# Kernel optimization log

Measured on AMD Instinct MI355X. Metric: run time of the kernel, lower is better.

## Reference

```python
import math
import jax, jax.numpy as jnp
import numpy as np

N_HEADS = 16
THETA = 10000.0


def _rope_cos_sin(S, head_dim):
    half = head_dim // 2
    inv_freq = 1.0 / (THETA ** (jnp.arange(half, dtype=jnp.float32) / half))
    t = jnp.arange(S, dtype=jnp.float32)
    freqs = t[:, None] * inv_freq[None, :]  # [S, half]
    return jnp.cos(freqs), jnp.sin(freqs)


def _apply_rope(x, cos, sin):
    # x: [B, H, S, D] float32; cos/sin: [S, D//2]
    half = x.shape[-1] // 2
    x1, x2 = x[..., :half], x[..., half:]
    c = cos[None, None, :, :]
    s = sin[None, None, :, :]
    return jnp.concatenate([x1 * c - x2 * s, x1 * s + x2 * c], axis=-1)


def setup_inputs() -> dict:
    key = jax.random.key(0)
    k1, k2, k3 = jax.random.split(key, 3)
    B, S, D = 4, 2048, 1024
    x = jax.random.normal(k1, (B, S, D), dtype=jnp.float32)
    w_qkv = jax.random.normal(k2, (3 * D, D), dtype=jnp.float32) * (1.0 / math.sqrt(D))
    w_out = jax.random.normal(k3, (D, D), dtype=jnp.float32) * (1.0 / math.sqrt(D))
    return {"x": x, "w_qkv": w_qkv, "w_out": w_out}


def reference(x, w_qkv, w_out):
    B, S, D = x.shape
    H = N_HEADS
    hd = D // H

    qkv = x @ w_qkv.T  # [B, S, 3D]
    q, k, v = jnp.split(qkv, 3, axis=-1)

    def reshape(t):
        return t.reshape(B, S, H, hd).transpose(0, 2, 1, 3)  # [B,H,S,hd]

    q, k, v = reshape(q), reshape(k), reshape(v)

    cos, sin = _rope_cos_sin(S, hd)
    q = _apply_rope(q.astype(jnp.float32), cos, sin).astype(x.dtype)
    k = _apply_rope(k.astype(jnp.float32), cos, sin).astype(x.dtype)

    scale = math.sqrt(hd)
    scores = jnp.einsum("bhsd,bhtd->bhst", q, k) / scale  # [B,H,S,S]
    causal = jnp.tril(jnp.ones((S, S), dtype=bool))
    scores = jnp.where(causal[None, None], scores, -jnp.inf)
    attn = jax.nn.softmax(scores.astype(jnp.float32), axis=-1).astype(x.dtype)

    out = jnp.einsum("bhst,bhtd->bhsd", attn, v)  # [B,H,S,hd]
    out = out.transpose(0, 2, 1, 3).reshape(B, S, D)
    return out @ w_out.T
```

## Files before the change

kernel.cpp:

```cpp
#include <hip/hip_runtime.h>
#include <hip/hip_bf16.h>

#define DEV static __device__ __forceinline__

typedef unsigned short u16;
typedef unsigned int u32;
typedef __attribute__((ext_vector_type(8))) short short8;
typedef __attribute__((ext_vector_type(4))) float f32x4;
typedef __attribute__((ext_vector_type(16))) float f32x16;
typedef __attribute__((ext_vector_type(4))) u32 u32x4;

static constexpr int Bsz = 4, Ssz = 2048, Dsz = 1024, Hn = 16, HD = 64;
static constexpr int Mrows = Bsz * Ssz;

DEV u16 f2bu(float f) {
  union { float f; u32 u; } a; a.f = f;
  u32 u = a.u;
  u32 r = (u + 0x7FFFu + ((u >> 16) & 1u)) >> 16;
  return (u16)r;
}
DEV float b2f(u16 v) {
  union { u32 u; float f; } a; a.u = ((u32)v) << 16;
  return a.f;
}
DEV u32 pk2(float lo, float hi2) {
  __hip_bfloat162 t = __float22bfloat162_rn(make_float2(lo, hi2));
  u32 r; __builtin_memcpy(&r, &t, 4); return r;
}
DEV f32x16 mfma3232(short8 a, short8 b, f32x16 c) {
  return __builtin_amdgcn_mfma_f32_32x32x16_bf16(a, b, c, 0, 0, 0);
}
DEV float max3f(float a, float b, float c) { return fmaxf(fmaxf(a, b), c); }
DEV float ex2(float x) { return __builtin_amdgcn_exp2f(x); }

__global__ void k_cast(const float4* __restrict__ in, ushort4* __restrict__ out, int n4) {
  int stride = gridDim.x * blockDim.x;
  for (int i = blockIdx.x * blockDim.x + threadIdx.x; i < n4; i += stride) {
    float4 v = in[i];
    ushort4 o;
    o.x = f2bu(v.x); o.y = f2bu(v.y); o.z = f2bu(v.z); o.w = f2bu(v.w);
    out[i] = o;
  }
}

__global__ void k_ropetab(float2* __restrict__ cst) {
  int i = blockIdx.x * blockDim.x + threadIdx.x;
  if (i >= Ssz * 32) return;
  int s = i >> 5, d = i & 31;
  float inv = powf(10000.0f, -(float)d / 32.0f);
  float fr = (float)s * inv;
  cst[i] = make_float2(cosf(fr), sinf(fr));
}

DEV void cp16(const u16* g, u16* l) {
  __builtin_amdgcn_global_load_lds((const __attribute__((address_space(1))) u32*)g,
                                   (__attribute__((address_space(3))) u32*)l, 16, 0, 0);
}

template <bool OUTBF16>
__global__ __launch_bounds__(256, 2) void k_gemm(const u16* __restrict__ A,
                                                 const u16* __restrict__ W,
                                                 void* __restrict__ C, int N, int K,
                                                 const float2* __restrict__ cst, int cpx,
                                                 u16* __restrict__ vtp) {
  __shared__ __align__(16) u16 SMEM[32768];
  const int tid = threadIdx.x;
  const int wid = tid >> 6, lane = tid & 63;
  const int lr = lane & 15, u = lane >> 4;
  const int wm = wid >> 1, wn = wid & 1;

  const int wg = blockIdx.x;
  const int xcd = wg & 7;
  const int j = wg >> 3;
  const int brow = (j / cpx) * 128;
  const int bcol = (xcd * cpx + j % cpx) * 128;

  const int rw = wid * 32 + (lane >> 3);
  const int octS = ((lane & 7) ^ (rw & 7)) * 8;
  const u16* aS = A + (size_t)(brow + rw) * K + octS;
  const u16* bS = W + (size_t)(bcol + rw) * K + octS;
  const int dBase = wid * 2048 + lane * 8;

  const int aBase = (wm * 64 + lr) * 64;
  const int bBase = (wn * 64 + lr) * 64;
  const int o0 = (u ^ (lane & 7)) * 8;
  const int o1 = ((4 + u) ^ (lane & 7)) * 8;

  f32x4 acc[4][4];
#pragma unroll
  for (int i = 0; i < 4; ++i)
#pragma unroll
    for (int j2 = 0; j2 < 4; ++j2) acc[i][j2] = (f32x4){0.f, 0.f, 0.f, 0.f};

  const int nt = K >> 6;

#define STG(kk, bb)                                                    \
  do {                                                                 \
    u16* ad = SMEM + (bb)*8192 + dBase;                                \
    u16* bd = SMEM + 16384 + (bb)*8192 + dBase;                        \
    cp16(aS + (kk), ad);                                               \
    cp16(aS + (size_t)8 * K + (kk), ad + 512);                         \
    cp16(aS + (size_t)16 * K + (kk), ad + 1024);                       \
    cp16(aS + (size_t)24 * K + (kk), ad + 1536);                       \
    cp16(bS + (kk), bd);                                               \
    cp16(bS + (size_t)8 * K + (kk), bd + 512);                         \
    cp16(bS + (size_t)16 * K + (kk), bd + 1024);                       \
    cp16(bS + (size_t)24 * K + (kk), bd + 1536);                       \
  } while (0)

  STG(0, 0);

  for (int t = 0; t < nt; ++t) {
    asm volatile("s_waitcnt vmcnt(0)" ::: "memory");
    __builtin_amdgcn_s_barrier();
    if (t + 1 < nt) STG((t + 1) << 6, (t + 1) & 1);
    const u16* ab = SMEM + (t & 1) * 8192;
    const u16* bb = SMEM + 16384 + (t & 1) * 8192;
    short8 a0[4], a1[4], b0[4], b1[4];
#pragma unroll
    for (int mr = 0; mr < 4; ++mr) {
      a0[mr] = *(const short8*)(ab + aBase + mr * 1024 + o0);
      a1[mr] = *(const short8*)(ab + aBase + mr * 1024 + o1);
    }
#pragma unroll
    for (int nr = 0; nr < 4; ++nr) {
      b0[nr] = *(const short8*)(bb + bBase + nr * 1024 + o0);
      b1[nr] = *(const short8*)(bb + bBase + nr * 1024 + o1);
    }
    __builtin_amdgcn_s_setprio(1);
#pragma unroll
    for (int mr = 0; mr < 4; ++mr)
#pragma unroll
      for (int nr = 0; nr < 4; ++nr)
        acc[mr][nr] =
            __builtin_amdgcn_mfma_f32_16x16x32_bf16(a0[mr], b0[nr], acc[mr][nr], 0, 0, 0);
#pragma unroll
    for (int mr = 0; mr < 4; ++mr)
#pragma unroll
      for (int nr = 0; nr < 4; ++nr)
        acc[mr][nr] =
            __builtin_amdgcn_mfma_f32_16x16x32_bf16(a1[mr], b1[nr], acc[mr][nr], 0, 0, 0);
    __builtin_amdgcn_s_setprio(0);
  }
#undef STG

  if (OUTBF16) {
    __syncthreads();
    const int rmode = (bcol < 1024) ? 0 : (bcol < 2048) ? 1 : 2;
    if (rmode < 2) {
      const float sc = (rmode == 0) ? 0.18033688f : 1.0f;
#pragma unroll
      for (int mr = 0; mr < 4; ++mr)
#pragma unroll
        for (int r = 0; r < 4; ++r) {
          const int row = wm * 64 + mr * 16 + u * 4 + r;
          const int s = (brow + row) & 2047;
          const float2 c0 = cst[s * 32 + lr];
          const float2 c1 = cst[s * 32 + 16 + lr];
          const float x10 = acc[mr][0][r], x11 = acc[mr][1][r];
          const float x20 = acc[mr][2][r], x21 = acc[mr][3][r];
          u16* lp = SMEM + row * 136 + wn * 64 + lr;
          lp[0]  = f2bu((x10 * c0.x - x20 * c0.y) * sc);
          lp[16] = f2bu((x11 * c1.x - x21 * c1.y) * sc);
          lp[32] = f2bu((x10 * c0.y + x20 * c0.x) * sc);
          lp[48] = f2bu((x11 * c1.y + x21 * c1.x) * sc);
        }
      __syncthreads();
      u16* cp = (u16*)C;
#pragma unroll
      for (int i = 0; i < 8; ++i) {
        const int e = i * 2048 + tid * 8;
        const int row = e >> 7, col = e & 127;
        short8 v = *(const short8*)(SMEM + row * 136 + col);
        *(short8*)(cp + (size_t)(brow + row) * N + bcol + col) = v;
      }
    } else {
#pragma unroll
      for (int mr = 0; mr < 4; ++mr)
#pragma unroll
        for (int nr = 0; nr < 4; ++nr)
#pragma unroll
          for (int r = 0; r < 4; ++r) {
            const int dl = wn * 64 + nr * 16 + lr;
            const int sl = wm * 64 + mr * 16 + u * 4 + r;
            SMEM[dl * 136 + sl] = f2bu(acc[mr][nr][r]);
          }
      __syncthreads();
      const int bb2 = brow >> 11;
      const int sbase = brow & 2047;
#pragma unroll
      for (int i = 0; i < 8; ++i) {
        const int e = i * 2048 + tid * 8;
        const int dl = e >> 7, sl = e & 127;
        const int gd = (bcol - 2048) + dl;
        short8 v = *(const short8*)(SMEM + dl * 136 + sl);
        *(short8*)(vtp + (size_t)(bb2 * 1024 + gd) * 2048 + sbase + sl) = v;
      }
    }
  } else {
    const int row0 = brow + wm * 64 + u * 4;
    const int col0 = bcol + wn * 64 + lr;
#pragma unroll
    for (int mr = 0; mr < 4; ++mr)
#pragma unroll
      for (int r = 0; r < 4; ++r) {
        size_t base = (size_t)(row0 + mr * 16 + r) * N + col0;
#pragma unroll
        for (int nr = 0; nr < 4; ++nr) ((float*)C)[base + nr * 16] = acc[mr][nr][r];
      }
  }
}

__global__ __launch_bounds__(256, 4) void k_attn(const u16* __restrict__ qkv,
                                                 const u16* __restrict__ vt,
                                                 u16* __restrict__ obuf) {
  __shared__ __align__(16) u16 Ksm[2][64 * 64];
  __shared__ __align__(16) u16 Vsm[2][64 * 64];

  const int tid = threadIdx.x;
  const int wid = tid >> 6;
  const int lane = tid & 63;
  const int l31 = lane & 31;
  const int hi = lane >> 5;
  const int r7 = l31 & 7;

  const int fid = blockIdx.x;
  const int a = fid & 3, bq = (fid >> 8) & 3;
  const int bh = (fid >> 2) & 63;
  const int sel = a ^ bq;
  const int qt = (sel == 0) ? bq : (sel == 1) ? 7 - bq : (sel == 2) ? 8 + bq : 15 - bq;

  const int b = bh >> 4;
  const int h = bh & 15;

  const float NEG = -__builtin_inff();

  const int srow = lane >> 3;
  const int scol = ((lane & 7) ^ srow) * 8;
  const u16* ksrc0 = qkv + (size_t)(b * Ssz + wid * 16 + srow) * 3072 + 1024 + h * 64 + scol;
  const u16* ksrc1 = ksrc0 + (size_t)8 * 3072;
  const u16* vsrc0 = vt + ((size_t)bh * 64 + wid * 16 + srow) * Ssz + scol;
  const u16* vsrc1 = vsrc0 + (size_t)8 * Ssz;
  u16* kD0 = Ksm[0] + wid * 1024;
  u16* vD0 = Vsm[0] + wid * 1024;

  const int q0 = qt * 128;
  const int qrow = q0 + (wid << 5) + l31;

  const u16* qptr = qkv + (size_t)(b * Ssz + qrow) * 3072 + h * 64 + hi * 8;
  short8 qf[4];
#pragma unroll
  for (int s = 0; s < 4; ++s) qf[s] = *(const short8*)(qptr + s * 16);

  f32x16 o0 = {0.f}, o1 = {0.f};
  float m = NEG, lsum = 0.f;

  const int ntiles = 2 * qt + 2;
  const int lastT = 2 * qt + (wid >> 1);

  cp16(ksrc0, kD0);
  cp16(ksrc1, kD0 + 512);
  cp16(vsrc0, vD0);
  cp16(vsrc1, vD0 + 512);

  const u16* kS0 = ksrc0 + (size_t)64 * 3072;
  const u16* kS1 = ksrc1 + (size_t)64 * 3072;
  const u16* vS0 = vsrc0 + 64;
  const u16* vS1 = vsrc1 + 64;

  for (int t = 0; t < ntiles; ++t) {
    __syncthreads();
    if (t + 1 < ntiles) {
      const int nb = (t + 1) & 1;
      cp16(kS0, kD0 + nb * 4096);
      cp16(kS1, kD0 + nb * 4096 + 512);
      cp16(vS0, vD0 + nb * 4096);
      cp16(vS1, vD0 + nb * 4096 + 512);
      kS0 += (size_t)64 * 3072;
      kS1 += (size_t)64 * 3072;
      vS0 += 64;
      vS1 += 64;
    }
    if (t > lastT) continue;

    const u16* kbuf = Ksm[t & 1];
    const u16* vbuf = Vsm[t & 1];
    const int kv0 = t << 6;

    f32x16 st0 = {0.f}, st1 = {0.f};
    __builtin_amdgcn_s_setprio(1);
#pragma unroll
    for (int s = 0; s < 4; ++s) {
      const int slot = (((2 * s + hi) ^ r7) << 3);
      short8 k0 = *(const short8*)(kbuf + l31 * 64 + slot);
      short8 k1 = *(const short8*)(kbuf + (32 + l31) * 64 + slot);
      st0 = mfma3232(k0, qf[s], st0);
      st1 = mfma3232(k1, qf[s], st1);
    }
    __builtin_amdgcn_s_setprio(0);

    if (t == lastT) {
      const int kb0 = kv0 + 4 * hi;
#pragma unroll
      for (int r = 0; r < 16; ++r) {
        const int ko = (r & 3) + 8 * (r >> 2);
        if (kb0 + ko > qrow) st0[r] = NEG;
        if (kb0 + 32 + ko > qrow) st1[r] = NEG;
      }
    }

    float c0 = max3f(st0[0], st0[1], st0[2]);
    c0 = max3f(c0, st0[3], st1[0]);
    c0 = max3f(c0, st1[1], st1[2]);
    c0 = fmaxf(c0, st1[3]);
    float c1 = max3f(st0[4], st0[5], st0[6]);
    c1 = max3f(c1, st0[7], st1[4]);
    c1 = max3f(c1, st1[5], st1[6]);
    c1 = fmaxf(c1, st1[7]);
    float c2 = max3f(st0[8], st0[9], st0[10]);
    c2 = max3f(c2, st0[11], st1[8]);
    c2 = max3f(c2, st1[9], st1[10]);
    c2 = fmaxf(c2, st1[11]);
    float c3 = max3f(st0[12], st0[13], st0[14]);
    c3 = max3f(c3, st0[15], st1[12]);
    c3 = max3f(c3, st1[13], st1[14]);
    c3 = fmaxf(c3, st1[15]);
    float pm = fmaxf(max3f(c0, c1, c2), c3);
    pm = fmaxf(pm, __shfl_xor(pm, 32));

    if (!__all(pm <= m + 8.0f)) {
      const float mn = fmaxf(m, pm);
      const float corr = ex2(m - mn);
      lsum *= corr;
      o0 *= corr;
      o1 *= corr;
      m = mn;
    }

    float rsp[4] = {0.f, 0.f, 0.f, 0.f};
#pragma unroll
    for (int r = 0; r < 16; ++r) {
      const float p0 = ex2(st0[r] - m);
      const float p1 = ex2(st1[r] - m);
      st0[r] = p0;
      st1[r] = p1;
      rsp[r & 3] += p0 + p1;
    }
    float rs = (rsp[0] + rsp[1]) + (rsp[2] + rsp[3]);
    rs += __shfl_xor(rs, 32);
    lsum += rs;

    u32 wa[8], wb[8];
#pragma unroll
    for (int g = 0; g < 4; ++g) {
      wa[g] = pk2(st0[4 * g + 0], st0[4 * g + 1]);
      wb[g] = pk2(st0[4 * g + 2], st0[4 * g + 3]);
      wa[4 + g] = pk2(st1[4 * g + 0], st1[4 * g + 1]);
      wb[4 + g] = pk2(st1[4 * g + 2], st1[4 * g + 3]);
    }

#pragma unroll
    for (int s = 0; s < 4; ++s) {
      const u32 uA0 = wa[2 * s], uA1 = wa[2 * s + 1];
      const u32 uB0 = wb[2 * s], uB1 = wb[2 * s + 1];
      const u32 tA0 = __shfl_xor(uA0, 32), tA1 = __shfl_xor(uA1, 32);
      const u32 tB0 = __shfl_xor(uB0, 32), tB1 = __shfl_xor(uB1, 32);
      u32x4 pw;
      pw.x = hi ? tA1 : uA0;
      pw.y = hi ? tB1 : uB0;
      pw.z = hi ? uA1 : tA0;
      pw.w = hi ? uB1 : tB0;
      short8 pfrag = *(short8*)&pw;
      const int slot = (((2 * s + hi) ^ r7) << 3);
      short8 v0 = *(const short8*)(vbuf + l31 * 64 + slot);
      short8 v1 = *(const short8*)(vbuf + (32 + l31) * 64 + slot);
      __builtin_amdgcn_s_setprio(1);
      o0 = mfma3232(v0, pfrag, o0);
      o1 = mfma3232(v1, pfrag, o1);
      __builtin_amdgcn_s_setprio(0);
    }
  }

  const float inv = 1.0f / lsum;
  u16* orow = obuf + (size_t)(b * Ssz + qrow) * 1024 + h * 64;
#pragma unroll
  for (int j = 0; j < 4; ++j) {
    ushort4 s0, s1;
    s0.x = f2bu(o0[4 * j + 0] * inv);
    s0.y = f2bu(o0[4 * j + 1] * inv);
    s0.z = f2bu(o0[4 * j + 2] * inv);
    s0.w = f2bu(o0[4 * j + 3] * inv);
    s1.x = f2bu(o1[4 * j + 0] * inv);
    s1.y = f2bu(o1[4 * j + 1] * inv);
    s1.z = f2bu(o1[4 * j + 2] * inv);
    s1.w = f2bu(o1[4 * j + 3] * inv);
    *(ushort4*)(orow + 8 * j + 4 * hi) = s0;
    *(ushort4*)(orow + 32 + 8 * j + 4 * hi) = s1;
  }
}

extern "C" void kernel_launch(void* const* d_in, const int* in_sizes, int n_in,
                              void* d_out, int out_size, void* d_ws, size_t ws_size,
                              hipStream_t stream) {
  const float* x = (const float*)d_in[0];
  const float* wqkv = (const float*)d_in[1];
  const float* wout = (const float*)d_in[2];

  char* ws = (char*)d_ws;
  u16* xb      = (u16*)(ws + 0);
  u16* wqkvb   = (u16*)(ws + 16777216);
  u16* woutb   = (u16*)(ws + 23068672);
  u16* qkv     = (u16*)(ws + 25165824);
  u16* vt      = (u16*)(ws + 75497472);
  u16* obuf    = (u16*)(ws + 92274688);
  float2* cst  = (float2*)(ws + 109051904);

  k_cast<<<2048, 256, 0, stream>>>((const float4*)x, (ushort4*)xb, Mrows * Dsz / 4);
  k_cast<<<2048, 256, 0, stream>>>((const float4*)wqkv, (ushort4*)wqkvb, 3 * Dsz * Dsz / 4);
  k_cast<<<1024, 256, 0, stream>>>((const float4*)wout, (ushort4*)woutb, Dsz * Dsz / 4);
  k_ropetab<<<256, 256, 0, stream>>>(cst);

  k_gemm<true><<<1536, 256, 0, stream>>>(xb, wqkvb, qkv, 3072, 1024, cst, 3, vt);

  k_attn<<<1024, 256, 0, stream>>>(qkv, vt, obuf);

  k_gemm<false><<<512, 256, 0, stream>>>(obuf, woutb, d_out, 1024, 1024, nullptr, 1, nullptr);
}
```

Baseline: 179.3 us.

## Enlarge attention blocks to 256 query rows and stage output GEMM stores

The attention kernel now runs 512-thread blocks covering 256 query rows. Eight waves share each double-buffered 64-row K/V tile, which halves the number of blocks reloading the same keys and values, and query tiles are remapped for causal balance. Separately, the fp32 output projection epilogue writes accumulators to padded shared memory and then stores coalesced float4 rows instead of scattered scalar stores. The risks are higher register pressure under the new launch bounds, coarser load balance with only 512 attention blocks, and an extra shared-memory pass plus barriers in the GEMM epilogue.

Result: no change. 182.3 us (+1.7%).

```diff
diff --git a/kernel.cpp b/kernel.cpp
--- a/kernel.cpp
+++ b/kernel.cpp
@@ -63,7 +63,7 @@
                                                  void* __restrict__ C, int N, int K,
                                                  const float2* __restrict__ cst, int cpx,
                                                  u16* __restrict__ vtp) {
-  __shared__ __align__(16) u16 SMEM[32768];
+  __shared__ __align__(16) u16 SMEM[33792];
   const int tid = threadIdx.x;
   const int wid = tid >> 6, lane = tid & 63;
   const int lr = lane & 15, u = lane >> 4;
@@ -198,20 +198,29 @@
       }
     }
   } else {
-    const int row0 = brow + wm * 64 + u * 4;
-    const int col0 = bcol + wn * 64 + lr;
+    __syncthreads();
+    float* FS = (float*)SMEM;
 #pragma unroll
     for (int mr = 0; mr < 4; ++mr)
 #pragma unroll
-      for (int r = 0; r < 4; ++r) {
-        size_t base = (size_t)(row0 + mr * 16 + r) * N + col0;
-#pragma unroll
-        for (int nr = 0; nr < 4; ++nr) ((float*)C)[base + nr * 16] = acc[mr][nr][r];
-      }
+      for (int nr = 0; nr < 4; ++nr)
+#pragma unroll
+        for (int r = 0; r < 4; ++r)
+          FS[(wm * 64 + mr * 16 + u * 4 + r) * 132 + wn * 64 + nr * 16 + lr] =
+              acc[mr][nr][r];
+    __syncthreads();
+    float* cp = (float*)C;
+#pragma unroll
+    for (int i = 0; i < 16; ++i) {
+      const int e = i * 1024 + tid * 4;
+      const int row = e >> 7, col = e & 127;
+      float4 v = *(const float4*)(FS + row * 132 + col);
+      *(float4*)(cp + (size_t)(brow + row) * N + bcol + col) = v;
+    }
   }
 }
 
-__global__ __launch_bounds__(256, 4) void k_attn(const u16* __restrict__ qkv,
+__global__ __launch_bounds__(512, 4) void k_attn(const u16* __restrict__ qkv,
                                                  const u16* __restrict__ vt,
                                                  u16* __restrict__ obuf) {
   __shared__ __align__(16) u16 Ksm[2][64 * 64];
@@ -225,10 +234,9 @@
   const int r7 = l31 & 7;
 
   const int fid = blockIdx.x;
-  const int a = fid & 3, bq = (fid >> 8) & 3;
-  const int bh = (fid >> 2) & 63;
-  const int sel = a ^ bq;
-  const int qt = (sel == 0) ? bq : (sel == 1) ? 7 - bq : (sel == 2) ? 8 + bq : 15 - bq;
+  const int bh = fid & 63;
+  const int e = (fid >> 6) & 7;
+  const int qt = (e < 4) ? e : (7 - (e & 3));
 
   const int b = bh >> 4;
   const int h = bh & 15;
@@ -237,14 +245,12 @@
 
   const int srow = lane >> 3;
   const int scol = ((lane & 7) ^ srow) * 8;
-  const u16* ksrc0 = qkv + (size_t)(b * Ssz + wid * 16 + srow) * 3072 + 1024 + h * 64 + scol;
-  const u16* ksrc1 = ksrc0 + (size_t)8 * 3072;
-  const u16* vsrc0 = vt + ((size_t)bh * 64 + wid * 16 + srow) * Ssz + scol;
-  const u16* vsrc1 = vsrc0 + (size_t)8 * Ssz;
-  u16* kD0 = Ksm[0] + wid * 1024;
-  u16* vD0 = Vsm[0] + wid * 1024;
-
-  const int q0 = qt * 128;
+  const u16* ksrc = qkv + (size_t)(b * Ssz + wid * 8 + srow) * 3072 + 1024 + h * 64 + scol;
+  const u16* vsrc = vt + ((size_t)bh * 64 + wid * 8 + srow) * Ssz + scol;
+  u16* kD0 = Ksm[0] + wid * 512;
+  u16* vD0 = Vsm[0] + wid * 512;
+
+  const int q0 = qt * 256;
   const int qrow = q0 + (wid << 5) + l31;
 
   const u16* qptr = qkv + (size_t)(b * Ssz + qrow) * 3072 + h * 64 + hi * 8;
@@ -255,31 +261,23 @@
   f32x16 o0 = {0.f}, o1 = {0.f};
   float m = NEG, lsum = 0.f;
 
-  const int ntiles = 2 * qt + 2;
-  const int lastT = 2 * qt + (wid >> 1);
-
-  cp16(ksrc0, kD0);
-  cp16(ksrc1, kD0 + 512);
-  cp16(vsrc0, vD0);
-  cp16(vsrc1, vD0 + 512);
-
-  const u16* kS0 = ksrc0 + (size_t)64 * 3072;
-  const u16* kS1 = ksrc1 + (size_t)64 * 3072;
-  const u16* vS0 = vsrc0 + 64;
-  const u16* vS1 = vsrc1 + 64;
+  const int ntiles = 4 * qt + 4;
+  const int lastT = 4 * qt + (wid >> 1);
+
+  cp16(ksrc, kD0);
+  cp16(vsrc, vD0);
+
+  const u16* kS = ksrc + (size_t)64 * 3072;
+  const u16* vS = vsrc + 64;
 
   for (int t = 0; t < ntiles; ++t) {
     __syncthreads();
     if (t + 1 < ntiles) {
       const int nb = (t + 1) & 1;
-      cp16(kS0, kD0 + nb * 4096);
-      cp16(kS1, kD0 + nb * 4096 + 512);
-      cp16(vS0, vD0 + nb * 4096);
-      cp16(vS1, vD0 + nb * 4096 + 512);
-      kS0 += (size_t)64 * 3072;
-      kS1 += (size_t)64 * 3072;
-      vS0 += 64;
-      vS1 += 64;
+      cp16(kS, kD0 + nb * 4096);
+      cp16(vS, vD0 + nb * 4096);
+      kS += (size_t)64 * 3072;
+      vS += 64;
     }
     if (t > lastT) continue;
 
@@ -422,7 +420,7 @@
 
   k_gemm<true><<<1536, 256, 0, stream>>>(xb, wqkvb, qkv, 3072, 1024, cst, 3, vt);
 
-  k_attn<<<1024, 256, 0, stream>>>(qkv, vt, obuf);
+  k_attn<<<512, 512, 0, stream>>>(qkv, vt, obuf);
 
   k_gemm<false><<<512, 256, 0, stream>>>(obuf, woutb, d_out, 1024, 1024, nullptr, 1, nullptr);
 }
```
